# Kernel optimization log

Measured on AMD Instinct MI355X. Metric: run time of the kernel, lower is better.

## Reference

```python
import jax, jax.numpy as jnp
import numpy as np

L = 3
NUM_NODES = 4000
NUM_RELS = 200
V = 20
EMB = 128
HID = 128
OUT = 100
N = 50000
E = 800000
B = 32
DECAY = 0.03


def setup_inputs() -> dict:
    key = jax.random.key(0)
    ks = jax.random.split(key, 20)
    s = 0.05  # weight scale
    inp = {
        'node_emb': jax.random.normal(ks[0], (NUM_NODES, EMB), jnp.float32) * s,
        'rel_emb': jax.random.normal(ks[1], (NUM_RELS, EMB), jnp.float32) * s,
        'lin_w': jax.random.normal(ks[2], (HID, EMB), jnp.float32) * s,  # torch Linear weight [out,in]
        'lin_b': jnp.zeros((HID,), jnp.float32),
        'alpha_w': jax.random.normal(ks[3], (L, NUM_NODES, NUM_NODES), jnp.float32) * 0.01,
        'alpha_b': jnp.zeros((L, NUM_NODES), jnp.float32),
        'beta_w': jax.random.normal(ks[4], (L, NUM_NODES), jnp.float32) * 0.01,
        'beta_b': jnp.zeros((L,), jnp.float32),
        'wr_w': jax.random.normal(ks[5], (L, HID), jnp.float32) * s,
        'wr_b': jnp.zeros((L,), jnp.float32),
        'conv_w': jax.random.normal(ks[6], (L, HID, HID), jnp.float32) * s,
        'conv_b': jnp.zeros((L, HID), jnp.float32),
        'mlp_w': jax.random.normal(ks[7], (OUT, 2 * HID), jnp.float32) * s,
        'mlp_b': jnp.zeros((OUT,), jnp.float32),
        'visit_node': jax.random.uniform(ks[8], (B, V, NUM_NODES), jnp.float32),
        'ehr_nodes': jax.random.uniform(ks[9], (B, NUM_NODES), jnp.float32),
        'node_ids': jax.random.randint(ks[10], (N,), 0, NUM_NODES, jnp.int32),
        'rel_ids': jax.random.randint(ks[11], (E,), 0, NUM_RELS, jnp.int32),
        'edge_index': jax.random.randint(ks[12], (2, E), 0, N, jnp.int32),
        'batch': jnp.sort(jax.random.randint(ks[13], (N,), 0, B, jnp.int32)),
    }
    return inp


def reference(node_emb, rel_emb, lin_w, lin_b, alpha_w, alpha_b, beta_w, beta_b,
              wr_w, wr_b, conv_w, conv_b, mlp_w, mlp_b, visit_node, ehr_nodes,
              node_ids, rel_ids, edge_index, batch):
    # initial node / edge features
    x = node_emb[node_ids] @ lin_w.T + lin_b                # [N, HID]
    edge_attr = rel_emb[rel_ids] @ lin_w.T + lin_b          # [E, HID]

    # temporal decay per visit: lambda_j = exp(decay*(V - j)), shape [1, V, 1]
    j = jnp.arange(V, dtype=jnp.float32)
    lam = jnp.exp(DECAY * (V - j))[None, :, None]

    src = edge_index[0]
    dst = edge_index[1]
    xj_nid = node_ids[src]                                  # [E]
    xj_bat = batch[src]                                     # [E]

    for l in range(L):
        # alpha: softmax over the visit axis (dim=1)
        alpha = jax.nn.softmax(
            jnp.einsum('bvn,mn->bvm', visit_node, alpha_w[l]) + alpha_b[l], axis=1)
        beta = jnp.tanh(
            jnp.einsum('bvn,n->bv', visit_node, beta_w[l])[:, :, None] + beta_b[l]) * lam
        attn = jnp.sum(alpha * beta, axis=1)                # [B, NUM_NODES]
        e_attn = attn[xj_bat, xj_nid][:, None]              # [E, 1]

        # BiAttentionGNNConv message + add-aggregate
        w_rel = edge_attr @ wr_w[l][:, None] + wr_b[l]      # [E, 1]
        msg = jax.nn.relu(x[src] * e_attn + w_rel * edge_attr)
        agg = jax.ops.segment_sum(msg, dst, num_segments=N)
        out = agg + x                                       # eps = 0 -> (1+eps)=1
        x = out @ conv_w[l].T + conv_b[l]                   # conv.nn Linear
        x = jax.nn.relu(x)                                  # outer F.relu (dropout inactive in eval)

    # global mean pool over graphs
    cnt = jax.ops.segment_sum(jnp.ones((N,), x.dtype), batch, num_segments=B)
    x_graph = jax.ops.segment_sum(x, batch, num_segments=B) / jnp.maximum(cnt, 1.0)[:, None]

    # patient node embedding branch
    x_node = (ehr_nodes @ node_emb) / jnp.sum(ehr_nodes, axis=1, keepdims=True)
    x_node = x_node @ lin_w.T + lin_b                       # [B, HID]

    logits = jnp.concatenate([x_graph, x_node], axis=1) @ mlp_w.T + mlp_b
    return logits
```

## Files before the change

kernel.cpp:

```cpp
#include <hip/hip_runtime.h>
#include <hip/hip_bf16.h>
#include <stdint.h>

#define LL      3
#define NNODES  4000
#define NRELS   200
#define VV      20
#define EMB     128
#define HIDD    128
#define OUTD    100
#define WS_N    50000
#define WS_E    800000
#define BV      32
#define DECAYF  0.03f
#define AK      4032
#define ZSTRIDE ((long)LL*640*4000)
#define SCAN_NB 196

typedef __bf16 bf16x8 __attribute__((ext_vector_type(8)));
typedef __bf16 bf16x4 __attribute__((ext_vector_type(4)));
typedef __bf16 bf16x2 __attribute__((ext_vector_type(2)));
typedef float  f32x4  __attribute__((ext_vector_type(4)));

__device__ __forceinline__ void glds16(const __bf16* g, __bf16* l) {
    __builtin_amdgcn_global_load_lds((const __attribute__((address_space(1))) void*)g,
                                     (__attribute__((address_space(3))) void*)l, 16, 0, 0);
}

__global__ __launch_bounds__(256) void k_cvt2(const float* __restrict__ visit,
                                              const float* __restrict__ alpha_w,
                                              __bf16* __restrict__ visit_bf,
                                              __bf16* __restrict__ alpha_bf) {
    long bid = blockIdx.x;
    const float* ip; __bf16* op;
    if (bid < BV*VV) { ip = visit + bid*4000; op = visit_bf + bid*AK; }
    else             { long r = bid - BV*VV; ip = alpha_w + r*4000; op = alpha_bf + r*AK; }
    int t = threadIdx.x;
    if (t < 250) {
        const float4* p4 = (const float4*)ip + t*4;
        float4 f0 = p4[0], f1 = p4[1], f2 = p4[2], f3 = p4[3];
        bf16x8 h0, h1;
        h0[0]=(__bf16)f0.x; h0[1]=(__bf16)f0.y; h0[2]=(__bf16)f0.z; h0[3]=(__bf16)f0.w;
        h0[4]=(__bf16)f1.x; h0[5]=(__bf16)f1.y; h0[6]=(__bf16)f1.z; h0[7]=(__bf16)f1.w;
        h1[0]=(__bf16)f2.x; h1[1]=(__bf16)f2.y; h1[2]=(__bf16)f2.z; h1[3]=(__bf16)f2.w;
        h1[4]=(__bf16)f3.x; h1[5]=(__bf16)f3.y; h1[6]=(__bf16)f3.z; h1[7]=(__bf16)f3.w;
        ((bf16x8*)op)[t*2]   = h0;
        ((bf16x8*)op)[t*2+1] = h1;
    } else if (t < 254) {
        bf16x8 zz;
        #pragma unroll
        for (int j = 0; j < 8; j++) zz[j] = (__bf16)0.f;
        ((bf16x8*)op)[500 + (t - 250)] = zz;
    }
}

__global__ __launch_bounds__(256)
void gemm_alpha(const __bf16* __restrict__ visit_bf, const __bf16* __restrict__ alpha_bf,
                __bf16* __restrict__ zpart)
{
    __shared__ __bf16 Ah[128*64];
    __shared__ __bf16 Bh[128*64];

    const int id   = blockIdx.x;
    const int xcd  = id & 7;
    const int slot = id >> 3;
    const int mi   = slot % 5;
    const int gix  = slot / 5;
    const int g    = xcd * 48 + gix;
    const int ni   = g & 31;
    const int lkh  = g >> 5;
    const int l    = lkh >> 2;
    const int kh   = lkh & 3;

    const __bf16* Ag = visit_bf;
    const __bf16* Bg = alpha_bf + (long)l * NNODES * AK;
    __bf16*       Cg = zpart + (long)kh * ZSTRIDE + (long)l * 640 * 4000;
    const int m0 = mi * 128;
    const int n0 = ni * 128;
    const int k0 = kh * 1024;
    const int k1 = (kh == 3) ? AK : (k0 + 1024);

    const int tid = threadIdx.x;
    const int wv  = tid >> 6;
    const int ln  = tid & 63;
    const int srow = ln >> 3;
    const int gsl  = (ln & 7) ^ srow;

    const __bf16* aA = Ag + (long)(m0 + wv*8 + srow) * AK + gsl*8;
    const __bf16* bB[4];
    #pragma unroll
    for (int t = 0; t < 4; t++) {
        int br = n0 + wv*8 + srow + t*32;
        if (br > NNODES-1) br = NNODES-1;
        bB[t] = Bg + (long)br * AK + gsl*8;
    }

    const int wm = (wv & 1) * 64;
    const int wn = (wv >> 1) * 64;
    const int lr = ln & 15;
    const int kq = ln >> 4;
    const int sw0 = lr & 7;

    f32x4 acc[4][4];
    #pragma unroll
    for (int i = 0; i < 4; i++)
        #pragma unroll
        for (int j = 0; j < 4; j++)
            acc[i][j] = (f32x4){0.f, 0.f, 0.f, 0.f};

    for (int kb = k0; kb < k1; kb += 64) {
        #pragma unroll
        for (int t = 0; t < 4; t++) {
            glds16(aA + (long)t*32*AK + kb, &Ah[(t*4 + wv) * 512]);
            glds16(bB[t] + kb,              &Bh[(t*4 + wv) * 512]);
        }
        __syncthreads();
        #pragma unroll
        for (int ks = 0; ks < 2; ks++) {
            const int sg = ((ks*4 + kq) ^ sw0) * 8;
            bf16x8 af[4], bfr[4];
            #pragma unroll
            for (int i = 0; i < 4; i++) {
                af[i]  = *(const bf16x8*)&Ah[(wm + i*16 + lr)*64 + sg];
                bfr[i] = *(const bf16x8*)&Bh[(wn + i*16 + lr)*64 + sg];
            }
            #pragma unroll
            for (int i = 0; i < 4; i++)
                #pragma unroll
                for (int j = 0; j < 4; j++)
                    acc[i][j] = __builtin_amdgcn_mfma_f32_16x16x32_bf16(af[i], bfr[j], acc[i][j], 0, 0, 0);
        }
        __syncthreads();
    }

    #pragma unroll
    for (int i = 0; i < 4; i++) {
        const int row_b = m0 + wm + i*16 + kq*4;
        #pragma unroll
        for (int j = 0; j < 4; j++) {
            const int col = n0 + wn + j*16 + lr;
            if (col < NNODES) {
                #pragma unroll
                for (int r = 0; r < 4; r++)
                    Cg[(long)(row_b + r)*4000 + col] = (__bf16)acc[i][j][r];
            }
        }
    }
}

#define BM 128
#define BN 128
#define BKG 32
#define LSTR 40

template<int SPLIT>
__device__ __forceinline__ void stage_tile(const float* __restrict__ G, int rows, int Kdim,
                                           int r0, int kb, int k1, __bf16* Sh, __bf16* Sl, int tid)
{
    const int sr  = tid >> 1;
    const int skc = (tid & 1) * 16;
    const int gr  = r0 + sr;
    const int gk  = kb + skc;
    float va[16];
    if (gr < rows && gk + 16 <= k1) {
        const float4* p4 = (const float4*)(G + (long)gr * Kdim + gk);
        #pragma unroll
        for (int q = 0; q < 4; q++) {
            float4 f = p4[q];
            va[4*q+0] = f.x; va[4*q+1] = f.y; va[4*q+2] = f.z; va[4*q+3] = f.w;
        }
    } else {
        #pragma unroll
        for (int j = 0; j < 16; j++) {
            int kk = gk + j;
            va[j] = (gr < rows && kk < k1) ? G[(long)gr * Kdim + kk] : 0.0f;
        }
    }
    bf16x8 h[2], lo[2];
    #pragma unroll
    for (int half = 0; half < 2; half++) {
        #pragma unroll
        for (int j = 0; j < 8; j++) {
            float v = va[half*8 + j];
            __bf16 hi = (__bf16)v;
            h[half][j]  = hi;
            lo[half][j] = (__bf16)(v - (float)hi);
        }
    }
    *(bf16x8*)&Sh[sr*LSTR + skc]     = h[0];
    *(bf16x8*)&Sh[sr*LSTR + skc + 8] = h[1];
    if (SPLIT) {
        *(bf16x8*)&Sl[sr*LSTR + skc]     = lo[0];
        *(bf16x8*)&Sl[sr*LSTR + skc + 8] = lo[1];
    }
}

template<int SPLIT, int RELU, int BIAS, int WRITEB>
__global__ __launch_bounds__(256)
void gemm_bt(const float* __restrict__ Ag, const float* __restrict__ Bg,
             float* __restrict__ Cg, const float* __restrict__ bias,
             __bf16* __restrict__ Xb, int M, int N, int K)
{
    __shared__ __bf16 Ah[BM*LSTR];
    __shared__ __bf16 Bh[BN*LSTR];
    __shared__ __bf16 Alo[SPLIT ? BM*LSTR : 1];
    __shared__ __bf16 Blo[SPLIT ? BN*LSTR : 1];

    const int tid = threadIdx.x;
    const int m0 = blockIdx.x * BM;
    const int n0 = blockIdx.y * BN;

    const int wave = tid >> 6;
    const int lane = tid & 63;
    const int wm = (wave & 1) * 64;
    const int wn = (wave >> 1) * 64;
    const int lr = lane & 15;
    const int kq = lane >> 4;

    f32x4 acc[4][4];
    #pragma unroll
    for (int i = 0; i < 4; i++)
        #pragma unroll
        for (int j = 0; j < 4; j++)
            acc[i][j] = (f32x4){0.f, 0.f, 0.f, 0.f};

    for (int kb = 0; kb < K; kb += BKG) {
        stage_tile<SPLIT>(Ag, M, K, m0, kb, K, Ah, Alo, tid);
        stage_tile<SPLIT>(Bg, N, K, n0, kb, K, Bh, Blo, tid);
        __syncthreads();

        bf16x8 af[4], bfr[4];
        #pragma unroll
        for (int i = 0; i < 4; i++) {
            af[i]  = *(const bf16x8*)&Ah[(wm + i*16 + lr)*LSTR + kq*8];
            bfr[i] = *(const bf16x8*)&Bh[(wn + i*16 + lr)*LSTR + kq*8];
        }
        #pragma unroll
        for (int i = 0; i < 4; i++)
            #pragma unroll
            for (int j = 0; j < 4; j++)
                acc[i][j] = __builtin_amdgcn_mfma_f32_16x16x32_bf16(af[i], bfr[j], acc[i][j], 0, 0, 0);

        if (SPLIT) {
            bf16x8 al[4], bl[4];
            #pragma unroll
            for (int i = 0; i < 4; i++) {
                al[i] = *(const bf16x8*)&Alo[(wm + i*16 + lr)*LSTR + kq*8];
                bl[i] = *(const bf16x8*)&Blo[(wn + i*16 + lr)*LSTR + kq*8];
            }
            #pragma unroll
            for (int i = 0; i < 4; i++)
                #pragma unroll
                for (int j = 0; j < 4; j++) {
                    acc[i][j] = __builtin_amdgcn_mfma_f32_16x16x32_bf16(af[i], bl[j], acc[i][j], 0, 0, 0);
                    acc[i][j] = __builtin_amdgcn_mfma_f32_16x16x32_bf16(al[i], bfr[j], acc[i][j], 0, 0, 0);
                }
        }
        __syncthreads();
    }

    #pragma unroll
    for (int i = 0; i < 4; i++) {
        const int row_b = m0 + wm + i*16 + kq*4;
        #pragma unroll
        for (int j = 0; j < 4; j++) {
            const int col = n0 + wn + j*16 + lr;
            if (col < N) {
                #pragma unroll
                for (int r = 0; r < 4; r++) {
                    const int row = row_b + r;
                    if (row < M) {
                        float v = acc[i][j][r];
                        if (BIAS) v += bias[col];
                        if (RELU) v = fmaxf(v, 0.0f);
                        Cg[(long)row*N + col] = v;
                        if (WRITEB) Xb[(long)row*N + col] = (__bf16)v;
                    }
                }
            }
        }
    }
}

__global__ void k_count(const int* __restrict__ dst, int* __restrict__ deg) {
    int e = blockIdx.x*256 + threadIdx.x;
    if (e < WS_E) atomicAdd(&deg[dst[e]], 1);
}

__global__ __launch_bounds__(256) void k_scan1(const int* __restrict__ deg, int* __restrict__ bsum) {
    __shared__ int red[256];
    int t = threadIdx.x;
    int i = blockIdx.x*256 + t;
    red[t] = (i < WS_N) ? deg[i] : 0;
    __syncthreads();
    for (int o = 128; o > 0; o >>= 1) {
        if (t < o) red[t] += red[t + o];
        __syncthreads();
    }
    if (t == 0) bsum[blockIdx.x] = red[0];
}

__global__ __launch_bounds__(256) void k_scan2(const int* __restrict__ bsum, int* __restrict__ bbase,
                                               int* __restrict__ offs) {
    __shared__ int s[256];
    int t = threadIdx.x;
    int v = (t < SCAN_NB) ? bsum[t] : 0;
    s[t] = v;
    __syncthreads();
    for (int o = 1; o < 256; o <<= 1) {
        int add = (t >= o) ? s[t - o] : 0;
        __syncthreads();
        s[t] += add;
        __syncthreads();
    }
    if (t < SCAN_NB) bbase[t] = s[t] - v;
    if (t == 0) offs[WS_N] = WS_E;
}

__global__ __launch_bounds__(256) void k_scan3(const int* __restrict__ deg, const int* __restrict__ bbase,
                                               int* __restrict__ offs, int* __restrict__ cursor) {
    __shared__ int s[256];
    int t = threadIdx.x;
    int i = blockIdx.x*256 + t;
    int v = (i < WS_N) ? deg[i] : 0;
    s[t] = v;
    __syncthreads();
    for (int o = 1; o < 256; o <<= 1) {
        int add = (t >= o) ? s[t - o] : 0;
        __syncthreads();
        s[t] += add;
        __syncthreads();
    }
    if (i < WS_N) {
        int e = bbase[blockIdx.x] + s[t] - v;
        offs[i] = e;
        cursor[i] = e;
    }
}

__global__ void k_fill(const int* __restrict__ dst, const int* __restrict__ src,
                       const int* __restrict__ rel, int* __restrict__ cursor,
                       int2* __restrict__ sr) {
    int e = blockIdx.x*256 + threadIdx.x;
    if (e < WS_E) {
        int d = dst[e];
        int p = atomicAdd(&cursor[d], 1);
        sr[p] = make_int2(src[e], rel[e]);
    }
}

__global__ __launch_bounds__(128) void k_relmsg(const float* __restrict__ Wrel, const float* __restrict__ wr_w,
                                                const float* __restrict__ wr_b, __bf16* __restrict__ relmsg) {
    int l = blockIdx.x / NRELS;
    int r = blockIdx.x % NRELS;
    int o = threadIdx.x;
    float wv = Wrel[r*HIDD + o];
    __shared__ float red[128];
    red[o] = wv * wr_w[l*HIDD + o];
    __syncthreads();
    for (int s = 64; s > 0; s >>= 1) {
        if (o < s) red[o] += red[o + s];
        __syncthreads();
    }
    float wrel = red[0] + wr_b[l];
    relmsg[((long)l*NRELS + r)*HIDD + o] = (__bf16)(wrel * wv);
}

__global__ void k_xinit(const float* __restrict__ Wnode, const int* __restrict__ nid,
                        const int* __restrict__ batch, const float* __restrict__ attn,
                        float* __restrict__ x, __bf16* __restrict__ xb, float* __restrict__ an) {
    int t = blockIdx.x*256 + threadIdx.x;
    if (t >= WS_N*32) return;
    int i = t >> 5;
    int d = t & 31;
    int n = nid[i];
    float4 v = ((const float4*)Wnode)[n*32 + d];
    ((float4*)x)[i*32 + d] = v;
    bf16x4 b;
    b[0] = (__bf16)v.x; b[1] = (__bf16)v.y; b[2] = (__bf16)v.z; b[3] = (__bf16)v.w;
    ((bf16x4*)xb)[i*32 + d] = b;
    if (d < LL) an[(long)d*WS_N + i] = attn[((long)d*BV + batch[i]) * NNODES + n];
}

__global__ __launch_bounds__(256) void k_beta(const float* __restrict__ visit, const float* __restrict__ beta_w,
                                              const float* __restrict__ beta_b, float* __restrict__ beta) {
    int id = blockIdx.x;
    int l = id / (BV*VV);
    int rem = id % (BV*VV);
    int b = rem / VV;
    int v = rem % VV;
    const float* row = visit + ((long)b*VV + v) * NNODES;
    const float* wr  = beta_w + (long)l * NNODES;
    float s = 0.f;
    for (int n = threadIdx.x; n < NNODES; n += 256) s += row[n] * wr[n];
    __shared__ float red[256];
    red[threadIdx.x] = s; __syncthreads();
    for (int o = 128; o > 0; o >>= 1) {
        if (threadIdx.x < o) red[threadIdx.x] += red[threadIdx.x + o];
        __syncthreads();
    }
    if (threadIdx.x == 0) {
        float lam = __expf(DECAYF * (float)(VV - v));
        beta[id] = tanhf(red[0] + beta_b[l]) * lam;
    }
}

__global__ __launch_bounds__(256) void k_attnpool(const __bf16* __restrict__ zpart,
                                                  const float* __restrict__ beta, float* __restrict__ attn) {
    int m = blockIdx.x*256 + threadIdx.x;
    int b = blockIdx.y;
    int l = blockIdx.z;
    if (m >= NNODES) return;
    const __bf16* zp = zpart + ((long)l*640 + b*VV) * 4000 + m;
    const float* bet = beta + (l*BV + b) * VV;
    float zv[VV];
    float mx = -1e30f;
    #pragma unroll
    for (int v = 0; v < VV; v++) {
        long o = (long)v * 4000;
        float s = (float)zp[o] + (float)zp[ZSTRIDE + o] + (float)zp[2*ZSTRIDE + o] + (float)zp[3*ZSTRIDE + o];
        zv[v] = s;
        mx = fmaxf(mx, s);
    }
    float s = 0.f, ws = 0.f;
    #pragma unroll
    for (int v = 0; v < VV; v++) {
        float e = __expf(zv[v] - mx);
        s += e;
        ws += e * bet[v];
    }
    attn[((long)l*BV + b) * NNODES + m] = ws / s;
}

__global__ __launch_bounds__(256) void k_agg(const float* __restrict__ x, const __bf16* __restrict__ xb,
                                             const float* __restrict__ an,
                                             const __bf16* __restrict__ relmsg_l, const int* __restrict__ offs,
                                             const int2* __restrict__ sr,
                                             float* __restrict__ outb) {
    int node = blockIdx.x*4 + (threadIdx.x >> 6);
    int lane = threadIdx.x & 63;
    if (node >= WS_N) return;
    int e0 = offs[node], e1 = offs[node + 1];
    const bf16x2* xb2 = (const bf16x2*)xb;
    const bf16x2* rm2 = (const bf16x2*)relmsg_l;
    float2 acc = {0.f, 0.f};
    int e = e0;
    for (; e + 8 <= e1; e += 8) {
        int2 p[8];
        #pragma unroll
        for (int q = 0; q < 8; q++) p[q] = sr[e + q];
        float a[8]; bf16x2 gv[8], mv[8];
        #pragma unroll
        for (int q = 0; q < 8; q++) a[q] = an[p[q].x];
        #pragma unroll
        for (int q = 0; q < 8; q++) gv[q] = xb2[p[q].x*64 + lane];
        #pragma unroll
        for (int q = 0; q < 8; q++) mv[q] = rm2[p[q].y*64 + lane];
        #pragma unroll
        for (int q = 0; q < 8; q++) {
            acc.x += fmaxf((float)gv[q][0]*a[q] + (float)mv[q][0], 0.f);
            acc.y += fmaxf((float)gv[q][1]*a[q] + (float)mv[q][1], 0.f);
        }
    }
    for (; e < e1; e++) {
        int2 pa = sr[e];
        float aa = an[pa.x];
        bf16x2 ga = xb2[pa.x*64 + lane];
        bf16x2 va = rm2[pa.y*64 + lane];
        acc.x += fmaxf((float)ga[0]*aa + (float)va[0], 0.f);
        acc.y += fmaxf((float)ga[1]*aa + (float)va[1], 0.f);
    }
    float2 xo = ((const float2*)x)[node*64 + lane];
    acc.x += xo.x; acc.y += xo.y;
    ((float2*)outb)[node*64 + lane] = acc;
}

__global__ __launch_bounds__(256) void k_pool_partial(const float* __restrict__ x,
                                                      const int* __restrict__ batch,
                                                      float* __restrict__ xgsum) {
    int r0 = blockIdx.x * 128;
    int d = threadIdx.x & 127;
    int rofs = threadIdx.x >> 7;
    int r1 = min(r0 + 128, WS_N);
    float acc = 0.f;
    int curb = -1;
    for (int i = r0 + rofs; i < r1; i += 2) {
        int b = batch[i];
        if (b != curb) {
            if (curb >= 0) atomicAdd(&xgsum[curb*HIDD + d], acc);
            acc = 0.f; curb = b;
        }
        acc += x[(long)i*HIDD + d];
    }
    if (curb >= 0) atomicAdd(&xgsum[curb*HIDD + d], acc);
}

__global__ __launch_bounds__(128) void k_ehrpool(const float* __restrict__ ehr,
                                                 const float* __restrict__ node_emb,
                                                 float* __restrict__ xnsum, float* __restrict__ esum) {
    int b = blockIdx.y;
    int c = blockIdx.x;
    int d = threadIdx.x;
    int n0 = c * (NNODES/16), n1 = n0 + (NNODES/16);
    float acc = 0.f;
    for (int n = n0; n < n1; n++) {
        acc += ehr[b*NNODES + n] * node_emb[(long)n*HIDD + d];
    }
    atomicAdd(&xnsum[b*HIDD + d], acc);
    float s = 0.f;
    for (int n = n0 + d; n < n1; n += 128) s += ehr[b*NNODES + n];
    __shared__ float red[128];
    red[d] = s; __syncthreads();
    for (int o = 64; o > 0; o >>= 1) {
        if (d < o) red[d] += red[d + o];
        __syncthreads();
    }
    if (d == 0) atomicAdd(&esum[b], red[0]);
}

__global__ __launch_bounds__(128) void k_head(const float* __restrict__ xgsum,
                                              const float* __restrict__ xnsum,
                                              const float* __restrict__ esum,
                                              const int* __restrict__ batch,
                                              const float* __restrict__ lin_w, const float* __restrict__ lin_b,
                                              const float* __restrict__ mlp_w, const float* __restrict__ mlp_b,
                                              float* __restrict__ out) {
    int b = blockIdx.x;
    int d = threadIdx.x;
    int lo = 0, hi = WS_N;
    while (lo < hi) { int mid = (lo + hi) >> 1; if (batch[mid] < b) lo = mid + 1; else hi = mid; }
    int s0 = lo;
    lo = 0; hi = WS_N;
    while (lo < hi) { int mid = (lo + hi) >> 1; if (batch[mid] < b + 1) lo = mid + 1; else hi = mid; }
    int cnt = max(lo - s0, 1);
    __shared__ float t1[128];
    __shared__ float cat[2*HIDD];
    t1[d]  = xnsum[b*HIDD + d] / esum[b];
    cat[d] = xgsum[b*HIDD + d] / (float)cnt;
    __syncthreads();
    float o2 = lin_b[d];
    for (int k2 = 0; k2 < HIDD; k2++) o2 += t1[k2] * lin_w[d*HIDD + k2];
    cat[HIDD + d] = o2;
    __syncthreads();
    if (d < OUTD) {
        float a = mlp_b[d];
        for (int j = 0; j < 2*HIDD; j++) a += cat[j] * mlp_w[d*2*HIDD + j];
        out[b*OUTD + d] = a;
    }
}

extern "C" void kernel_launch(void* const* d_in, const int* in_sizes, int n_in,
                              void* d_out, int out_size, void* d_ws, size_t ws_size,
                              hipStream_t stream)
{
    const float* node_emb = (const float*)d_in[0];
    const float* rel_emb  = (const float*)d_in[1];
    const float* lin_w    = (const float*)d_in[2];
    const float* lin_b    = (const float*)d_in[3];
    const float* alpha_w  = (const float*)d_in[4];
    const float* beta_w   = (const float*)d_in[6];
    const float* beta_b   = (const float*)d_in[7];
    const float* wr_w     = (const float*)d_in[8];
    const float* wr_b     = (const float*)d_in[9];
    const float* conv_w   = (const float*)d_in[10];
    const float* conv_b   = (const float*)d_in[11];
    const float* mlp_w    = (const float*)d_in[12];
    const float* mlp_b    = (const float*)d_in[13];
    const float* visit    = (const float*)d_in[14];
    const float* ehr      = (const float*)d_in[15];
    const int* node_ids   = (const int*)d_in[16];
    const int* rel_ids    = (const int*)d_in[17];
    const int* ei         = (const int*)d_in[18];
    const int* batch      = (const int*)d_in[19];
    const int* esrc = ei;
    const int* edst = ei + WS_E;
    float* out = (float*)d_out;

    char* p = (char*)d_ws;
    auto take = [&](size_t bytes) -> char* {
        char* q = p;
        p += (bytes + 255) & ~(size_t)255;
        return q;
    };
    __bf16* zpart    = (__bf16*)take((size_t)4*ZSTRIDE*2);
    __bf16* visit_bf = (__bf16*)take((size_t)(BV*VV)*AK*2);
    char*   big      = take((size_t)LL*NNODES*AK*2);
    float* betab  = (float*)take((size_t)LL*BV*VV*4);
    float* xgsum  = (float*)take((size_t)BV*HIDD*4);
    float* xnsum  = (float*)take((size_t)BV*HIDD*4);
    float* esum   = (float*)take((size_t)BV*4);
    size_t small_zero_bytes = (size_t)((char*)(esum + BV) - (char*)xgsum);
    int* deg      = (int*)take((size_t)WS_N*4);
    int* offs     = (int*)take((size_t)(WS_N+1)*4);
    int* cursor   = (int*)take((size_t)WS_N*4);
    int* bsum     = (int*)take((size_t)SCAN_NB*4);
    int* bbase    = (int*)take((size_t)SCAN_NB*4);
    if ((size_t)(p - (char*)d_ws) > ws_size) return;

    __bf16* alpha_bf = (__bf16*)big;
    char* q = big;
    auto carve = [&](size_t bytes) -> char* {
        char* r = q;
        q += (bytes + 255) & ~(size_t)255;
        return r;
    };
    float*  x      = (float*)carve((size_t)WS_N*HIDD*4);
    __bf16* xb     = (__bf16*)carve((size_t)WS_N*HIDD*2);
    int2*   sr     = (int2*)carve((size_t)WS_E*8);
    float*  attn   = (float*)carve((size_t)LL*BV*NNODES*4);
    float*  attnnd = (float*)carve((size_t)LL*WS_N*4);
    float*  Wnode  = (float*)carve((size_t)NNODES*HIDD*4);
    float*  Wrel   = (float*)carve((size_t)NRELS*HIDD*4);
    __bf16* relmsg = (__bf16*)carve((size_t)LL*NRELS*HIDD*2);
    float*  aggbuf = (float*)zpart;

    (void)hipMemsetAsync(deg, 0, (size_t)WS_N*4, stream);
    (void)hipMemsetAsync(xgsum, 0, small_zero_bytes, stream);

    k_cvt2<<<dim3(BV*VV + LL*NNODES), 256, 0, stream>>>(visit, alpha_w, visit_bf, alpha_bf);
    gemm_alpha<<<dim3(1920), 256, 0, stream>>>(visit_bf, alpha_bf, zpart);
    k_beta<<<dim3(LL*BV*VV), 256, 0, stream>>>(visit, beta_w, beta_b, betab);
    k_attnpool<<<dim3((NNODES+255)/256, BV, LL), 256, 0, stream>>>(zpart, betab, attn);

    k_count<<<dim3((WS_E+255)/256), 256, 0, stream>>>(edst, deg);
    k_scan1<<<dim3(SCAN_NB), 256, 0, stream>>>(deg, bsum);
    k_scan2<<<1, 256, 0, stream>>>(bsum, bbase, offs);
    k_scan3<<<dim3(SCAN_NB), 256, 0, stream>>>(deg, bbase, offs, cursor);
    k_fill<<<dim3((WS_E+255)/256), 256, 0, stream>>>(edst, esrc, rel_ids, cursor, sr);

    gemm_bt<1,0,1,0><<<dim3((NNODES+BM-1)/BM, 1, 1), 256, 0, stream>>>(
        node_emb, lin_w, Wnode, lin_b, nullptr, NNODES, HIDD, HIDD);
    gemm_bt<1,0,1,0><<<dim3((NRELS+BM-1)/BM, 1, 1), 256, 0, stream>>>(
        rel_emb, lin_w, Wrel, lin_b, nullptr, NRELS, HIDD, HIDD);
    k_relmsg<<<dim3(LL*NRELS), 128, 0, stream>>>(Wrel, wr_w, wr_b, relmsg);
    k_xinit<<<dim3((WS_N*32+255)/256), 256, 0, stream>>>(Wnode, node_ids, batch, attn, x, xb, attnnd);

    for (int l = 0; l < LL; l++) {
        k_agg<<<dim3((WS_N+3)/4), 256, 0, stream>>>(
            x, xb, attnnd + (size_t)l*WS_N, relmsg + (size_t)l*NRELS*HIDD, offs, sr, aggbuf);
        gemm_bt<1,1,1,1><<<dim3((WS_N+BM-1)/BM, 1, 1), 256, 0, stream>>>(
            aggbuf, conv_w + (size_t)l*HIDD*HIDD, x, conv_b + (size_t)l*HIDD, xb,
            WS_N, HIDD, HIDD);
    }

    k_pool_partial<<<dim3((WS_N+127)/128), 256, 0, stream>>>(x, batch, xgsum);
    k_ehrpool<<<dim3(16, BV), 128, 0, stream>>>(ehr, node_emb, xnsum, esum);
    k_head<<<BV, 128, 0, stream>>>(xgsum, xnsum, esum, batch, lin_w, lin_b, mlp_w, mlp_b, out);
}
```

Measured before the change: 849.6 us.

## Fuse small kernels and restructure edge aggregation to process two edges per wave

Folds the beta dot product into the bf16 conversion kernel, merges the scan's middle pass into the final scan, fuses the relation linear into the relation-message kernel, and combines the two pooling kernels into one launch. It also merges the two memsets. Edge aggregation now splits each wave into halves that handle alternate edges with 4-wide bf16 loads and combine their sums with a shuffle. The intent is to cut launch count and redundant reads of visit. In exchange, each scan block redundantly rescans the block sums and the aggregation tail loop runs masked work.

```diff
diff --git a/kernel.cpp b/kernel.cpp
--- a/kernel.cpp
+++ b/kernel.cpp
@@ -16,6 +16,7 @@
 #define AK      4032
 #define ZSTRIDE ((long)LL*640*4000)
 #define SCAN_NB 196
+#define NPP     391
 
 typedef __bf16 bf16x8 __attribute__((ext_vector_type(8)));
 typedef __bf16 bf16x4 __attribute__((ext_vector_type(4)));
@@ -29,13 +30,18 @@
 
 __global__ __launch_bounds__(256) void k_cvt2(const float* __restrict__ visit,
                                               const float* __restrict__ alpha_w,
+                                              const float* __restrict__ beta_w,
+                                              const float* __restrict__ beta_b,
                                               __bf16* __restrict__ visit_bf,
-                                              __bf16* __restrict__ alpha_bf) {
+                                              __bf16* __restrict__ alpha_bf,
+                                              float* __restrict__ betab) {
     long bid = blockIdx.x;
+    const bool isv = bid < BV*VV;
     const float* ip; __bf16* op;
-    if (bid < BV*VV) { ip = visit + bid*4000; op = visit_bf + bid*AK; }
-    else             { long r = bid - BV*VV; ip = alpha_w + r*4000; op = alpha_bf + r*AK; }
+    if (isv) { ip = visit + bid*4000; op = visit_bf + bid*AK; }
+    else     { long r = bid - BV*VV; ip = alpha_w + r*4000; op = alpha_bf + r*AK; }
     int t = threadIdx.x;
+    float p0 = 0.f, p1 = 0.f, p2 = 0.f;
     if (t < 250) {
         const float4* p4 = (const float4*)ip + t*4;
         float4 f0 = p4[0], f1 = p4[1], f2 = p4[2], f3 = p4[3];
@@ -46,11 +52,39 @@
         h1[4]=(__bf16)f3.x; h1[5]=(__bf16)f3.y; h1[6]=(__bf16)f3.z; h1[7]=(__bf16)f3.w;
         ((bf16x8*)op)[t*2]   = h0;
         ((bf16x8*)op)[t*2+1] = h1;
+        if (isv) {
+            #pragma unroll
+            for (int l = 0; l < LL; l++) {
+                const float4* bw = (const float4*)(beta_w + (long)l*4000) + t*4;
+                float4 b0 = bw[0], b1 = bw[1], b2 = bw[2], b3 = bw[3];
+                float s = f0.x*b0.x + f0.y*b0.y + f0.z*b0.z + f0.w*b0.w
+                        + f1.x*b1.x + f1.y*b1.y + f1.z*b1.z + f1.w*b1.w
+                        + f2.x*b2.x + f2.y*b2.y + f2.z*b2.z + f2.w*b2.w
+                        + f3.x*b3.x + f3.y*b3.y + f3.z*b3.z + f3.w*b3.w;
+                if (l == 0) p0 = s; else if (l == 1) p1 = s; else p2 = s;
+            }
+        }
     } else if (t < 254) {
         bf16x8 zz;
         #pragma unroll
         for (int j = 0; j < 8; j++) zz[j] = (__bf16)0.f;
         ((bf16x8*)op)[500 + (t - 250)] = zz;
+    }
+    if (isv) {
+        __shared__ float r0[256], r1[256], r2[256];
+        r0[t] = p0; r1[t] = p1; r2[t] = p2;
+        __syncthreads();
+        for (int o = 128; o > 0; o >>= 1) {
+            if (t < o) { r0[t] += r0[t+o]; r1[t] += r1[t+o]; r2[t] += r2[t+o]; }
+            __syncthreads();
+        }
+        if (t == 0) {
+            int v = (int)(bid % VV);
+            float lam = __expf(DECAYF * (float)(VV - v));
+            betab[0*BV*VV + bid] = tanhf(r0[0] + beta_b[0]) * lam;
+            betab[1*BV*VV + bid] = tanhf(r1[0] + beta_b[1]) * lam;
+            betab[2*BV*VV + bid] = tanhf(r2[0] + beta_b[2]) * lam;
+        }
     }
 }
 
@@ -300,27 +334,22 @@
     if (t == 0) bsum[blockIdx.x] = red[0];
 }
 
-__global__ __launch_bounds__(256) void k_scan2(const int* __restrict__ bsum, int* __restrict__ bbase,
-                                               int* __restrict__ offs) {
+__global__ __launch_bounds__(256) void k_scan3(const int* __restrict__ deg, const int* __restrict__ bsum,
+                                               int* __restrict__ offs, int* __restrict__ cursor) {
+    __shared__ int sb[256];
     __shared__ int s[256];
     int t = threadIdx.x;
-    int v = (t < SCAN_NB) ? bsum[t] : 0;
-    s[t] = v;
+    int bv = (t < SCAN_NB) ? bsum[t] : 0;
+    sb[t] = bv;
     __syncthreads();
     for (int o = 1; o < 256; o <<= 1) {
-        int add = (t >= o) ? s[t - o] : 0;
-        __syncthreads();
-        s[t] += add;
-        __syncthreads();
-    }
-    if (t < SCAN_NB) bbase[t] = s[t] - v;
-    if (t == 0) offs[WS_N] = WS_E;
-}
-
-__global__ __launch_bounds__(256) void k_scan3(const int* __restrict__ deg, const int* __restrict__ bbase,
-                                               int* __restrict__ offs, int* __restrict__ cursor) {
-    __shared__ int s[256];
-    int t = threadIdx.x;
+        int add = (t >= o) ? sb[t - o] : 0;
+        __syncthreads();
+        sb[t] += add;
+        __syncthreads();
+    }
+    int base = (blockIdx.x == 0) ? 0 : sb[blockIdx.x - 1];
+
     int i = blockIdx.x*256 + t;
     int v = (i < WS_N) ? deg[i] : 0;
     s[t] = v;
@@ -332,10 +361,11 @@
         __syncthreads();
     }
     if (i < WS_N) {
-        int e = bbase[blockIdx.x] + s[t] - v;
+        int e = base + s[t] - v;
         offs[i] = e;
         cursor[i] = e;
     }
+    if (blockIdx.x == 0 && t == 0) offs[WS_N] = WS_E;
 }
 
 __global__ void k_fill(const int* __restrict__ dst, const int* __restrict__ src,
@@ -349,21 +379,33 @@
     }
 }
 
-__global__ __launch_bounds__(128) void k_relmsg(const float* __restrict__ Wrel, const float* __restrict__ wr_w,
-                                                const float* __restrict__ wr_b, __bf16* __restrict__ relmsg) {
-    int l = blockIdx.x / NRELS;
-    int r = blockIdx.x % NRELS;
+__global__ __launch_bounds__(128) void k_relfused(const float* __restrict__ rel_emb,
+                                                  const float* __restrict__ lin_w,
+                                                  const float* __restrict__ lin_b,
+                                                  const float* __restrict__ wr_w,
+                                                  const float* __restrict__ wr_b,
+                                                  __bf16* __restrict__ relmsg) {
+    int r = blockIdx.x;
     int o = threadIdx.x;
-    float wv = Wrel[r*HIDD + o];
+    __shared__ float row[128];
     __shared__ float red[128];
-    red[o] = wv * wr_w[l*HIDD + o];
+    row[o] = rel_emb[(long)r*EMB + o];
     __syncthreads();
-    for (int s = 64; s > 0; s >>= 1) {
-        if (o < s) red[o] += red[o + s];
-        __syncthreads();
-    }
-    float wrel = red[0] + wr_b[l];
-    relmsg[((long)l*NRELS + r)*HIDD + o] = (__bf16)(wrel * wv);
+    float wv = lin_b[o];
+    #pragma unroll 4
+    for (int k = 0; k < EMB; k++) wv += row[k] * lin_w[(long)o*EMB + k];
+    #pragma unroll
+    for (int l = 0; l < LL; l++) {
+        red[o] = wv * wr_w[l*HIDD + o];
+        __syncthreads();
+        for (int s2 = 64; s2 > 0; s2 >>= 1) {
+            if (o < s2) red[o] += red[o + s2];
+            __syncthreads();
+        }
+        float wrel = red[0] + wr_b[l];
+        __syncthreads();
+        relmsg[((long)l*NRELS + r)*HIDD + o] = (__bf16)(wrel * wv);
+    }
 }
 
 __global__ void k_xinit(const float* __restrict__ Wnode, const int* __restrict__ nid,
@@ -382,29 +424,6 @@
     if (d < LL) an[(long)d*WS_N + i] = attn[((long)d*BV + batch[i]) * NNODES + n];
 }
 
-__global__ __launch_bounds__(256) void k_beta(const float* __restrict__ visit, const float* __restrict__ beta_w,
-                                              const float* __restrict__ beta_b, float* __restrict__ beta) {
-    int id = blockIdx.x;
-    int l = id / (BV*VV);
-    int rem = id % (BV*VV);
-    int b = rem / VV;
-    int v = rem % VV;
-    const float* row = visit + ((long)b*VV + v) * NNODES;
-    const float* wr  = beta_w + (long)l * NNODES;
-    float s = 0.f;
-    for (int n = threadIdx.x; n < NNODES; n += 256) s += row[n] * wr[n];
-    __shared__ float red[256];
-    red[threadIdx.x] = s; __syncthreads();
-    for (int o = 128; o > 0; o >>= 1) {
-        if (threadIdx.x < o) red[threadIdx.x] += red[threadIdx.x + o];
-        __syncthreads();
-    }
-    if (threadIdx.x == 0) {
-        float lam = __expf(DECAYF * (float)(VV - v));
-        beta[id] = tanhf(red[0] + beta_b[l]) * lam;
-    }
-}
-
 __global__ __launch_bounds__(256) void k_attnpool(const __bf16* __restrict__ zpart,
                                                   const float* __restrict__ beta, float* __restrict__ attn) {
     int m = blockIdx.x*256 + threadIdx.x;
@@ -438,84 +457,104 @@
                                              const int2* __restrict__ sr,
                                              float* __restrict__ outb) {
     int node = blockIdx.x*4 + (threadIdx.x >> 6);
+    if (node >= WS_N) return;
     int lane = threadIdx.x & 63;
-    if (node >= WS_N) return;
+    int half = lane >> 5;
+    int lh   = lane & 31;
     int e0 = offs[node], e1 = offs[node + 1];
-    const bf16x2* xb2 = (const bf16x2*)xb;
-    const bf16x2* rm2 = (const bf16x2*)relmsg_l;
-    float2 acc = {0.f, 0.f};
+    const bf16x4* xb4 = (const bf16x4*)xb;
+    const bf16x4* rm4 = (const bf16x4*)relmsg_l;
+    float a0 = 0.f, a1 = 0.f, a2 = 0.f, a3 = 0.f;
     int e = e0;
     for (; e + 8 <= e1; e += 8) {
-        int2 p[8];
-        #pragma unroll
-        for (int q = 0; q < 8; q++) p[q] = sr[e + q];
-        float a[8]; bf16x2 gv[8], mv[8];
-        #pragma unroll
-        for (int q = 0; q < 8; q++) a[q] = an[p[q].x];
-        #pragma unroll
-        for (int q = 0; q < 8; q++) gv[q] = xb2[p[q].x*64 + lane];
-        #pragma unroll
-        for (int q = 0; q < 8; q++) mv[q] = rm2[p[q].y*64 + lane];
-        #pragma unroll
-        for (int q = 0; q < 8; q++) {
-            acc.x += fmaxf((float)gv[q][0]*a[q] + (float)mv[q][0], 0.f);
-            acc.y += fmaxf((float)gv[q][1]*a[q] + (float)mv[q][1], 0.f);
-        }
-    }
-    for (; e < e1; e++) {
-        int2 pa = sr[e];
-        float aa = an[pa.x];
-        bf16x2 ga = xb2[pa.x*64 + lane];
-        bf16x2 va = rm2[pa.y*64 + lane];
-        acc.x += fmaxf((float)ga[0]*aa + (float)va[0], 0.f);
-        acc.y += fmaxf((float)ga[1]*aa + (float)va[1], 0.f);
-    }
-    float2 xo = ((const float2*)x)[node*64 + lane];
-    acc.x += xo.x; acc.y += xo.y;
-    ((float2*)outb)[node*64 + lane] = acc;
-}
-
-__global__ __launch_bounds__(256) void k_pool_partial(const float* __restrict__ x,
-                                                      const int* __restrict__ batch,
-                                                      float* __restrict__ xgsum) {
-    int r0 = blockIdx.x * 128;
-    int d = threadIdx.x & 127;
-    int rofs = threadIdx.x >> 7;
-    int r1 = min(r0 + 128, WS_N);
-    float acc = 0.f;
-    int curb = -1;
-    for (int i = r0 + rofs; i < r1; i += 2) {
-        int b = batch[i];
-        if (b != curb) {
-            if (curb >= 0) atomicAdd(&xgsum[curb*HIDD + d], acc);
-            acc = 0.f; curb = b;
-        }
-        acc += x[(long)i*HIDD + d];
-    }
-    if (curb >= 0) atomicAdd(&xgsum[curb*HIDD + d], acc);
-}
-
-__global__ __launch_bounds__(128) void k_ehrpool(const float* __restrict__ ehr,
-                                                 const float* __restrict__ node_emb,
-                                                 float* __restrict__ xnsum, float* __restrict__ esum) {
-    int b = blockIdx.y;
-    int c = blockIdx.x;
-    int d = threadIdx.x;
-    int n0 = c * (NNODES/16), n1 = n0 + (NNODES/16);
-    float acc = 0.f;
-    for (int n = n0; n < n1; n++) {
-        acc += ehr[b*NNODES + n] * node_emb[(long)n*HIDD + d];
-    }
-    atomicAdd(&xnsum[b*HIDD + d], acc);
-    float s = 0.f;
-    for (int n = n0 + d; n < n1; n += 128) s += ehr[b*NNODES + n];
-    __shared__ float red[128];
-    red[d] = s; __syncthreads();
-    for (int o = 64; o > 0; o >>= 1) {
-        if (d < o) red[d] += red[d + o];
-        __syncthreads();
-    }
-    if (d == 0) atomicAdd(&esum[b], red[0]);
+        int2 pe[4];
+        #pragma unroll
+        for (int q = 0; q < 4; q++) pe[q] = sr[e + 2*q + half];
+        float aq[4]; bf16x4 gv[4], mv[4];
+        #pragma unroll
+        for (int q = 0; q < 4; q++) aq[q] = an[pe[q].x];
+        #pragma unroll
+        for (int q = 0; q < 4; q++) gv[q] = xb4[pe[q].x*32 + lh];
+        #pragma unroll
+        for (int q = 0; q < 4; q++) mv[q] = rm4[pe[q].y*32 + lh];
+        #pragma unroll
+        for (int q = 0; q < 4; q++) {
+            a0 += fmaxf((float)gv[q][0]*aq[q] + (float)mv[q][0], 0.f);
+            a1 += fmaxf((float)gv[q][1]*aq[q] + (float)mv[q][1], 0.f);
+            a2 += fmaxf((float)gv[q][2]*aq[q] + (float)mv[q][2], 0.f);
+            a3 += fmaxf((float)gv[q][3]*aq[q] + (float)mv[q][3], 0.f);
+        }
+    }
+    for (; e < e1; e += 2) {
+        int ei = e + half;
+        bool vld = ei < e1;
+        int2 pe = sr[vld ? ei : e];
+        float aa = vld ? an[pe.x] : 0.f;
+        bf16x4 ga = xb4[pe.x*32 + lh];
+        bf16x4 va = rm4[pe.y*32 + lh];
+        float vm = vld ? 1.f : 0.f;
+        a0 += vm * fmaxf((float)ga[0]*aa + (float)va[0], 0.f);
+        a1 += vm * fmaxf((float)ga[1]*aa + (float)va[1], 0.f);
+        a2 += vm * fmaxf((float)ga[2]*aa + (float)va[2], 0.f);
+        a3 += vm * fmaxf((float)ga[3]*aa + (float)va[3], 0.f);
+    }
+    a0 += __shfl_xor(a0, 32);
+    a1 += __shfl_xor(a1, 32);
+    a2 += __shfl_xor(a2, 32);
+    a3 += __shfl_xor(a3, 32);
+    if (half == 0) {
+        float4 xo = ((const float4*)x)[node*32 + lh];
+        float4 r;
+        r.x = a0 + xo.x; r.y = a1 + xo.y; r.z = a2 + xo.z; r.w = a3 + xo.w;
+        ((float4*)outb)[node*32 + lh] = r;
+    }
+}
+
+__global__ __launch_bounds__(256) void k_pool(const float* __restrict__ x,
+                                              const int* __restrict__ batch,
+                                              const float* __restrict__ ehr,
+                                              const float* __restrict__ node_emb,
+                                              float* __restrict__ xgsum,
+                                              float* __restrict__ xnsum,
+                                              float* __restrict__ esum) {
+    if (blockIdx.x < NPP) {
+        int r0 = blockIdx.x * 128;
+        int d = threadIdx.x & 127;
+        int rofs = threadIdx.x >> 7;
+        int r1 = min(r0 + 128, WS_N);
+        float acc = 0.f;
+        int curb = -1;
+        for (int i = r0 + rofs; i < r1; i += 2) {
+            int b = batch[i];
+            if (b != curb) {
+                if (curb >= 0) atomicAdd(&xgsum[curb*HIDD + d], acc);
+                acc = 0.f; curb = b;
+            }
+            acc += x[(long)i*HIDD + d];
+        }
+        if (curb >= 0) atomicAdd(&xgsum[curb*HIDD + d], acc);
+    } else {
+        int id = blockIdx.x - NPP;
+        int b = id >> 4;
+        int c = id & 15;
+        int d = threadIdx.x;
+        int n0 = c * (NNODES/16), n1 = n0 + (NNODES/16);
+        __shared__ float red[256];
+        if (d < 128) {
+            float acc = 0.f;
+            for (int n = n0; n < n1; n++)
+                acc += ehr[b*NNODES + n] * node_emb[(long)n*HIDD + d];
+            atomicAdd(&xnsum[b*HIDD + d], acc);
+        }
+        float s = 0.f;
+        for (int n = n0 + d; n < n1; n += 256) s += ehr[b*NNODES + n];
+        red[d] = s; __syncthreads();
+        for (int o = 128; o > 0; o >>= 1) {
+            if (d < o) red[d] += red[d + o];
+            __syncthreads();
+        }
+        if (d == 0) atomicAdd(&esum[b], red[0]);
+    }
 }
 
 __global__ __launch_bounds__(128) void k_head(const float* __restrict__ xgsum,
@@ -589,12 +628,11 @@
     float* xgsum  = (float*)take((size_t)BV*HIDD*4);
     float* xnsum  = (float*)take((size_t)BV*HIDD*4);
     float* esum   = (float*)take((size_t)BV*4);
-    size_t small_zero_bytes = (size_t)((char*)(esum + BV) - (char*)xgsum);
     int* deg      = (int*)take((size_t)WS_N*4);
+    size_t zero_bytes = (size_t)((char*)(deg + WS_N) - (char*)xgsum);
     int* offs     = (int*)take((size_t)(WS_N+1)*4);
     int* cursor   = (int*)take((size_t)WS_N*4);
     int* bsum     = (int*)take((size_t)SCAN_NB*4);
-    int* bbase    = (int*)take((size_t)SCAN_NB*4);
     if ((size_t)(p - (char*)d_ws) > ws_size) return;
 
     __bf16* alpha_bf = (__bf16*)big;
@@ -610,29 +648,24 @@
     float*  attn   = (float*)carve((size_t)LL*BV*NNODES*4);
     float*  attnnd = (float*)carve((size_t)LL*WS_N*4);
     float*  Wnode  = (float*)carve((size_t)NNODES*HIDD*4);
-    float*  Wrel   = (float*)carve((size_t)NRELS*HIDD*4);
     __bf16* relmsg = (__bf16*)carve((size_t)LL*NRELS*HIDD*2);
     float*  aggbuf = (float*)zpart;
 
-    (void)hipMemsetAsync(deg, 0, (size_t)WS_N*4, stream);
-    (void)hipMemsetAsync(xgsum, 0, small_zero_bytes, stream);
-
-    k_cvt2<<<dim3(BV*VV + LL*NNODES), 256, 0, stream>>>(visit, alpha_w, visit_bf, alpha_bf);
+    (void)hipMemsetAsync(xgsum, 0, zero_bytes, stream);
+
+    k_cvt2<<<dim3(BV*VV + LL*NNODES), 256, 0, stream>>>(visit, alpha_w, beta_w, beta_b,
+                                                        visit_bf, alpha_bf, betab);
     gemm_alpha<<<dim3(1920), 256, 0, stream>>>(visit_bf, alpha_bf, zpart);
-    k_beta<<<dim3(LL*BV*VV), 256, 0, stream>>>(visit, beta_w, beta_b, betab);
     k_attnpool<<<dim3((NNODES+255)/256, BV, LL), 256, 0, stream>>>(zpart, betab, attn);
 
     k_count<<<dim3((WS_E+255)/256), 256, 0, stream>>>(edst, deg);
     k_scan1<<<dim3(SCAN_NB), 256, 0, stream>>>(deg, bsum);
-    k_scan2<<<1, 256, 0, stream>>>(bsum, bbase, offs);
-    k_scan3<<<dim3(SCAN_NB), 256, 0, stream>>>(deg, bbase, offs, cursor);
+    k_scan3<<<dim3(SCAN_NB), 256, 0, stream>>>(deg, bsum, offs, cursor);
     k_fill<<<dim3((WS_E+255)/256), 256, 0, stream>>>(edst, esrc, rel_ids, cursor, sr);
 
     gemm_bt<1,0,1,0><<<dim3((NNODES+BM-1)/BM, 1, 1), 256, 0, stream>>>(
         node_emb, lin_w, Wnode, lin_b, nullptr, NNODES, HIDD, HIDD);
-    gemm_bt<1,0,1,0><<<dim3((NRELS+BM-1)/BM, 1, 1), 256, 0, stream>>>(
-        rel_emb, lin_w, Wrel, lin_b, nullptr, NRELS, HIDD, HIDD);
-    k_relmsg<<<dim3(LL*NRELS), 128, 0, stream>>>(Wrel, wr_w, wr_b, relmsg);
+    k_relfused<<<dim3(NRELS), 128, 0, stream>>>(rel_emb, lin_w, lin_b, wr_w, wr_b, relmsg);
     k_xinit<<<dim3((WS_N*32+255)/256), 256, 0, stream>>>(Wnode, node_ids, batch, attn, x, xb, attnnd);
 
     for (int l = 0; l < LL; l++) {
@@ -643,7 +676,6 @@
             WS_N, HIDD, HIDD);
     }
 
-    k_pool_partial<<<dim3((WS_N+127)/128), 256, 0, stream>>>(x, batch, xgsum);
-    k_ehrpool<<<dim3(16, BV), 128, 0, stream>>>(ehr, node_emb, xnsum, esum);
+    k_pool<<<dim3(NPP + 16*BV), 256, 0, stream>>>(x, batch, ehr, node_emb, xgsum, xnsum, esum);
     k_head<<<BV, 128, 0, stream>>>(xgsum, xnsum, esum, batch, lin_w, lin_b, mlp_w, mlp_b, out);
 }
```

Measured after the change: 820.1 us. -3.5%, faster.
